# Performance work log

Hardware: AMD Instinct MI355X
Metric: run time of the kernel (lower is better)

The kernel has to match this reference:

```python
import jax, jax.numpy as jnp
import numpy as np

DIMS = (8, 8, 16, 16)   # 4D lattice, prod = 16384 sites
ND = len(DIMS)
N_IN = 4
N_OUT = 4
NC = 3
KERNEL_SIZE = 2
DILATION = 0
INIT_W = 1.0

W_IN = 2 * N_IN + 1                                  # 9
T_W = 2 * (N_IN * (KERNEL_SIZE - 1) * ND) + 1        # 33


def cconj(w):
    # swap matrix indices (axes 3,4) and negate imaginary part (last axis)
    wT = jnp.swapaxes(w, 3, 4)
    return wT * jnp.array([1.0, -1.0], dtype=w.dtype)


def complex_einsum(pattern, a, b, conj_a=1, conj_b=1):
    aR, aI = a[..., 0], conj_a * a[..., 1]
    bR, bI = b[..., 0], conj_b * b[..., 1]
    cR = jnp.einsum(pattern, aR, bR) - jnp.einsum(pattern, aI, bI)
    cI = jnp.einsum(pattern, aR, bI) + jnp.einsum(pattern, aI, bR)
    return jnp.stack((cR, cI), axis=-1)


def shift(a, axis, orientation):
    # dim 1 is flattened lattice; unflatten, roll along lattice axis, re-flatten
    o_s = a.shape
    n_s = (o_s[0],) + DIMS + o_s[2:]
    return jnp.roll(a.reshape(n_s), orientation, axis=axis + 1).reshape(o_s)


def transport(u, w, axis):
    # positive-orientation gauge transport: U w(x+mu) U^dagger
    ws = shift(w, axis, -1)
    ua = u[:, :, axis]                                 # [b, x, nc, nc, 2]
    wt = complex_einsum('bxij,bxwjk->bxwik', ua, ws)
    wt = complex_einsum('bxwij,bxkj->bxwik', wt, ua, conj_b=-1)
    return wt


def setup_inputs() -> dict:
    key = jax.random.key(0)
    k1, k2 = jax.random.split(key)
    n_sites = int(np.prod(DIMS))
    x = jax.random.normal(k1, (1, n_sites, ND + N_IN, NC, NC, 2), dtype=jnp.float32)
    std = INIT_W * np.sqrt(1.0 / (W_IN * T_W))
    weight = jax.random.normal(k2, (N_OUT, W_IN, T_W), dtype=jnp.float32) * std
    return {"x": x, "weight": weight}


def reference(x, weight):
    u, w = x[:, :, :ND], x[:, :, ND:]
    transported = []
    for axis in range(ND):
        wt = w
        for d in range(1, KERNEL_SIZE):
            for _ in range(DILATION + 1):
                wt = transport(u, wt, axis)
            transported.append(wt)
    t_w = jnp.concatenate(transported, axis=2)          # [b, x, n_in*(K-1)*ND, nc, nc, 2]

    w_full = jnp.concatenate([w, cconj(w)], axis=2)
    t_w_full = jnp.concatenate([t_w, cconj(t_w)], axis=2)

    # unit element channel
    unit = jnp.stack((jnp.eye(NC, dtype=x.dtype), jnp.zeros((NC, NC), dtype=x.dtype)), axis=-1)
    b, n_sites = x.shape[0], x.shape[1]
    unit_t = jnp.broadcast_to(unit[None, None, None], (b, n_sites, 1, NC, NC, 2))
    w_full = jnp.concatenate([w_full, unit_t], axis=2)       # [b, x, 9, nc, nc, 2]
    t_w_full = jnp.concatenate([t_w_full, unit_t], axis=2)   # [b, x, 33, nc, nc, 2]

    # bilinear gauge-covariant products, then weight contraction
    ww = complex_einsum('bxvij,bxwjk->bxvwik', w_full, t_w_full)  # [b, x, 9, 33, nc, nc, 2]
    w_out = jnp.einsum('uvw,bxvwijc->bxuijc', weight, ww)         # [b, x, n_out, nc, nc, 2]

    return jnp.concatenate([u, w_out], axis=2)
```

## Files before the change

### kernel.cpp

```cpp
#include <hip/hip_runtime.h>
#include <stdint.h>


#define SPB 16
#define TPB 256
#define NSITES 16384
#define TS2_SITE 146
#define NWGT 1188

__device__ __forceinline__ float2 pk_fma(float2 a, float2 b, float2 c){
    return make_float2(fmaf(a.x, b.x, c.x), fmaf(a.y, b.y, c.y));
}
__device__ __forceinline__ float2 spl(float s){ return make_float2(s, s); }
__device__ __forceinline__ float2 pn(float s){ return make_float2(s, -s); }
__device__ __forceinline__ float2 np(float s){ return make_float2(-s, s); }
__device__ __forceinline__ float2 swp(float2 a){ return make_float2(a.y, a.x); }

__device__ __forceinline__ int neigh(int s, int a){
    if (a == 3) return (s & ~15)        | ((s + 1)    & 15);
    if (a == 2) return (s & ~(15 << 4)) | ((s + 16)   & (15 << 4));
    if (a == 1) return (s & ~(7 << 8))  | ((s + 256)  & (7 << 8));
    return              (s & ~(7 << 11))| ((s + 2048) & (7 << 11));
}

__global__ __launch_bounds__(TPB, 2)
void gcm_fused(const float* __restrict__ xp,
               const float* __restrict__ wgt,
               float* __restrict__ outp)
{
    __shared__ float2 lt[SPB * TS2_SITE];
    __shared__ float wsm[NWGT];
    const float2* x2 = (const float2*)xp;
    float2* o2 = (float2*)outp;

    const int tid = threadIdx.x;
    const int g   = tid & 3;
    const int u   = (tid >> 2) & 3;
    const int sl  = tid >> 4;
    const int s   = blockIdx.x * SPB + sl;

    #pragma unroll 1
    for (int idx = tid; idx < NWGT; idx += TPB) wsm[idx] = wgt[idx];

    {
        const int a = u, i = g;
        float2 uc[9], wc[9];
        {
            const float2* up = x2 + (s * 8 + a) * 9;
            #pragma unroll
            for (int e = 0; e < 9; e++) uc[e] = up[e];
        }
        const int sn = neigh(s, a);
        {
            const float2* wp = x2 + (sn * 8 + 4 + i) * 9;
            #pragma unroll
            for (int e = 0; e < 9; e++) wc[e] = wp[e];
        }
        float2 t1[9];
        #pragma unroll
        for (int r = 0; r < 3; r++){
            #pragma unroll
            for (int k = 0; k < 3; k++){
                float2 acc = make_float2(0.f, 0.f);
                #pragma unroll
                for (int j = 0; j < 3; j++){
                    float2 a_ = uc[r*3+j], b_ = wc[j*3+k];
                    acc = pk_fma(spl(a_.x), b_, acc);
                    acc = pk_fma(np(a_.y), swp(b_), acc);
                }
                t1[r*3+k] = acc;
            }
        }
        float2* dst = &lt[sl * TS2_SITE + (a * 4 + i) * 9];
        #pragma unroll
        for (int r = 0; r < 3; r++){
            #pragma unroll
            for (int k = 0; k < 3; k++){
                float2 acc = make_float2(0.f, 0.f);
                #pragma unroll
                for (int j = 0; j < 3; j++){
                    float2 a_ = t1[r*3+j], b_ = uc[k*3+j];
                    acc = pk_fma(pn(a_.x), b_, acc);
                    acc = pk_fma(spl(a_.y), swp(b_), acc);
                }
                dst[r*3+k] = acc;
            }
        }
    }
    __syncthreads();

    if (g == 1){
        const float2* src = x2 + (s * 8 + u) * 9;
        float2* dst = o2 + (s * 8 + u) * 9;
        #pragma unroll
        for (int e = 0; e < 9; e++) dst[e] = src[e];
    }

    float2 M1[9], M2[9], cc[9];
    #pragma unroll
    for (int e = 0; e < 9; e++){
        M1[e] = make_float2(0.f, 0.f);
        M2[e] = make_float2(0.f, 0.f);
        cc[e] = make_float2(0.f, 0.f);
    }

    const float* wu  = wsm + u * 297;
    const float* wuA = wu + g * 33;
    const float* wuB = wu + (4 + g) * 33;
    const float* wu8 = wu + 8 * 33;

    const float2* tbase = &lt[sl * TS2_SITE];

    #pragma unroll 1
    for (int w16 = 0; w16 < 16; w16++){
        const float2* tp = tbase + w16 * 9;
        float2 tc[9];
        #pragma unroll
        for (int e = 0; e < 9; e++) tc[e] = tp[e];
        float a1 = wuA[w16], b1 = wuA[16 + w16];
        float a2 = wuB[w16], b2 = wuB[16 + w16];
        const bool mine = ((w16 >> 2) == g);
        float c8 = mine ? wu8[w16]      : 0.f;
        float d8 = mine ? wu8[16 + w16] : 0.f;
        #pragma unroll
        for (int i = 0; i < 3; i++){
            #pragma unroll
            for (int j = 0; j < 3; j++){
                const int e = i*3+j, eT = j*3+i;
                M1[e] = pk_fma(spl(a1), tc[e],  M1[e]);
                M1[e] = pk_fma(pn(b1),  tc[eT], M1[e]);
                M2[e] = pk_fma(spl(a2), tc[e],  M2[e]);
                M2[e] = pk_fma(pn(b2),  tc[eT], M2[e]);
                cc[e] = pk_fma(spl(c8), tc[e],  cc[e]);
                cc[e] = pk_fma(pn(d8),  tc[eT], cc[e]);
            }
        }
    }

    {
        float c1 = wuA[32], c2 = wuB[32];
        M1[0].x += c1; M1[4].x += c1; M1[8].x += c1;
        M2[0].x += c2; M2[4].x += c2; M2[8].x += c2;
        if (g == 0){
            float e8 = wu8[32];
            cc[0].x += e8; cc[4].x += e8; cc[8].x += e8;
        }
    }

    float2 wg[9];
    {
        const float2* wp = x2 + (s * 8 + 4 + g) * 9;
        #pragma unroll
        for (int e = 0; e < 9; e++) wg[e] = wp[e];
    }

    #pragma unroll
    for (int i = 0; i < 3; i++){
        #pragma unroll
        for (int k = 0; k < 3; k++){
            float2 acc = cc[i*3+k];
            #pragma unroll
            for (int j = 0; j < 3; j++){
                float2 a_ = wg[i*3+j];
                float2 m  = M1[j*3+k];
                acc = pk_fma(spl(a_.x), m,      acc);
                acc = pk_fma(np(a_.y),  swp(m), acc);
            }
            #pragma unroll
            for (int j = 0; j < 3; j++){
                float2 b_ = wg[j*3+i];
                float2 m  = M2[j*3+k];
                acc = pk_fma(spl(b_.x), m,      acc);
                acc = pk_fma(pn(b_.y),  swp(m), acc);
            }
            cc[i*3+k] = acc;
        }
    }

    #pragma unroll
    for (int e = 0; e < 9; e++){
        cc[e].x += __shfl_xor(cc[e].x, 1);
        cc[e].x += __shfl_xor(cc[e].x, 2);
        cc[e].y += __shfl_xor(cc[e].y, 1);
        cc[e].y += __shfl_xor(cc[e].y, 2);
    }
    if (g == 0){
        float2* dst = o2 + (s * 8 + 4 + u) * 9;
        #pragma unroll
        for (int e = 0; e < 9; e++) dst[e] = cc[e];
    }
}

extern "C" void kernel_launch(void* const* d_in, const int* in_sizes, int n_in,
                              void* d_out, int out_size, void* d_ws, size_t ws_size,
                              hipStream_t stream)
{
    const float* x = (const float*)d_in[0];
    const float* w = (const float*)d_in[1];
    float* out = (float*)d_out;
    dim3 grid(NSITES / SPB);
    dim3 block(TPB);
    hipLaunchKernelGGL(gcm_fused, grid, block, 0, stream, x, w, out);
}
```

Baseline: 76.83 us.

## Split per-output work across eight lanes per site and use native packed FMA

```diff
diff --git a/kernel.cpp b/kernel.cpp
--- a/kernel.cpp
+++ b/kernel.cpp
@@ -2,19 +2,32 @@
 #include <stdint.h>
 
 
-#define SPB 16
+typedef float v2f __attribute__((ext_vector_type(2)));
+
+#define SPB 8
 #define TPB 256
 #define NSITES 16384
 #define TS2_SITE 146
 #define NWGT 1188
 
-__device__ __forceinline__ float2 pk_fma(float2 a, float2 b, float2 c){
-    return make_float2(fmaf(a.x, b.x, c.x), fmaf(a.y, b.y, c.y));
-}
-__device__ __forceinline__ float2 spl(float s){ return make_float2(s, s); }
-__device__ __forceinline__ float2 pn(float s){ return make_float2(s, -s); }
-__device__ __forceinline__ float2 np(float s){ return make_float2(-s, s); }
-__device__ __forceinline__ float2 swp(float2 a){ return make_float2(a.y, a.x); }
+#if defined(__has_builtin)
+#if __has_builtin(__builtin_elementwise_fma)
+#define HAVE_EW_FMA 1
+#endif
+#endif
+
+__device__ __forceinline__ v2f pkfma(v2f a, v2f b, v2f c){
+#ifdef HAVE_EW_FMA
+    return __builtin_elementwise_fma(a, b, c);
+#else
+    v2f r; r.x = fmaf(a.x, b.x, c.x); r.y = fmaf(a.y, b.y, c.y); return r;
+#endif
+}
+__device__ __forceinline__ v2f spl(float s){ return (v2f){s, s}; }
+__device__ __forceinline__ v2f pn (float s){ return (v2f){s, -s}; }
+__device__ __forceinline__ v2f np (float s){ return (v2f){-s, s}; }
+__device__ __forceinline__ v2f swp(v2f a){ return __builtin_shufflevector(a, a, 1, 0); }
+__device__ __forceinline__ v2f zero2(){ return (v2f){0.f, 0.f}; }
 
 __device__ __forceinline__ int neigh(int s, int a){
     if (a == 3) return (s & ~15)        | ((s + 1)    & 15);
@@ -23,155 +36,162 @@
     return              (s & ~(7 << 11))| ((s + 2048) & (7 << 11));
 }
 
-__global__ __launch_bounds__(TPB, 2)
+__global__ __launch_bounds__(TPB, 3)
 void gcm_fused(const float* __restrict__ xp,
                const float* __restrict__ wgt,
                float* __restrict__ outp)
 {
-    __shared__ float2 lt[SPB * TS2_SITE];
+    __shared__ v2f lt[SPB * TS2_SITE];
     __shared__ float wsm[NWGT];
-    const float2* x2 = (const float2*)xp;
-    float2* o2 = (float2*)outp;
+    const v2f* x2 = (const v2f*)xp;
+    v2f* o2 = (v2f*)outp;
 
     const int tid = threadIdx.x;
-    const int g   = tid & 3;
-    const int u   = (tid >> 2) & 3;
-    const int sl  = tid >> 4;
+    const int h   = tid & 7;
+    const int u   = (tid >> 3) & 3;
+    const int sl  = tid >> 5;
     const int s   = blockIdx.x * SPB + sl;
+    const int g   = h & 3;
 
     #pragma unroll 1
     for (int idx = tid; idx < NWGT; idx += TPB) wsm[idx] = wgt[idx];
 
-    {
-        const int a = u, i = g;
-        float2 uc[9], wc[9];
+    if (h < 4){
+        v2f uc[9], wc[9];
         {
-            const float2* up = x2 + (s * 8 + a) * 9;
+            const v2f* up = x2 + (s * 8 + u) * 9;
             #pragma unroll
             for (int e = 0; e < 9; e++) uc[e] = up[e];
         }
-        const int sn = neigh(s, a);
+        const int sn = neigh(s, u);
         {
-            const float2* wp = x2 + (sn * 8 + 4 + i) * 9;
+            const v2f* wp = x2 + (sn * 8 + 4 + h) * 9;
             #pragma unroll
             for (int e = 0; e < 9; e++) wc[e] = wp[e];
         }
-        float2 t1[9];
+        v2f t1[9];
         #pragma unroll
         for (int r = 0; r < 3; r++){
             #pragma unroll
             for (int k = 0; k < 3; k++){
-                float2 acc = make_float2(0.f, 0.f);
+                v2f acc = zero2();
                 #pragma unroll
                 for (int j = 0; j < 3; j++){
-                    float2 a_ = uc[r*3+j], b_ = wc[j*3+k];
-                    acc = pk_fma(spl(a_.x), b_, acc);
-                    acc = pk_fma(np(a_.y), swp(b_), acc);
+                    v2f a_ = uc[r*3+j], b_ = wc[j*3+k];
+                    acc = pkfma(spl(a_.x), b_, acc);
+                    acc = pkfma(np(a_.y), swp(b_), acc);
                 }
                 t1[r*3+k] = acc;
             }
         }
-        float2* dst = &lt[sl * TS2_SITE + (a * 4 + i) * 9];
+        v2f* dst = &lt[sl * TS2_SITE + (u * 4 + h) * 9];
         #pragma unroll
         for (int r = 0; r < 3; r++){
             #pragma unroll
             for (int k = 0; k < 3; k++){
-                float2 acc = make_float2(0.f, 0.f);
+                v2f acc = zero2();
                 #pragma unroll
                 for (int j = 0; j < 3; j++){
-                    float2 a_ = t1[r*3+j], b_ = uc[k*3+j];
-                    acc = pk_fma(pn(a_.x), b_, acc);
-                    acc = pk_fma(spl(a_.y), swp(b_), acc);
+                    v2f a_ = t1[r*3+j], b_ = uc[k*3+j];
+                    acc = pkfma(pn(a_.x), b_, acc);
+                    acc = pkfma(spl(a_.y), swp(b_), acc);
                 }
                 dst[r*3+k] = acc;
             }
         }
+    } else if (h == 4){
+        const v2f* src = x2 + (s * 8 + u) * 9;
+        v2f* dst = o2 + (s * 8 + u) * 9;
+        #pragma unroll
+        for (int e = 0; e < 9; e++) dst[e] = src[e];
     }
     __syncthreads();
 
-    if (g == 1){
-        const float2* src = x2 + (s * 8 + u) * 9;
-        float2* dst = o2 + (s * 8 + u) * 9;
-        #pragma unroll
-        for (int e = 0; e < 9; e++) dst[e] = src[e];
-    }
-
-    float2 M1[9], M2[9], cc[9];
-    #pragma unroll
-    for (int e = 0; e < 9; e++){
-        M1[e] = make_float2(0.f, 0.f);
-        M2[e] = make_float2(0.f, 0.f);
-        cc[e] = make_float2(0.f, 0.f);
-    }
+    v2f M[9], cc[9];
+    #pragma unroll
+    for (int e = 0; e < 9; e++){ M[e] = zero2(); cc[e] = zero2(); }
 
     const float* wu  = wsm + u * 297;
-    const float* wuA = wu + g * 33;
-    const float* wuB = wu + (4 + g) * 33;
+    const float* wvh = wu + h * 33;
     const float* wu8 = wu + 8 * 33;
 
-    const float2* tbase = &lt[sl * TS2_SITE];
+    const v2f* tbase = &lt[sl * TS2_SITE];
 
     #pragma unroll 1
     for (int w16 = 0; w16 < 16; w16++){
-        const float2* tp = tbase + w16 * 9;
-        float2 tc[9];
+        const v2f* tp = tbase + w16 * 9;
+        v2f tc[9];
         #pragma unroll
         for (int e = 0; e < 9; e++) tc[e] = tp[e];
-        float a1 = wuA[w16], b1 = wuA[16 + w16];
-        float a2 = wuB[w16], b2 = wuB[16 + w16];
-        const bool mine = ((w16 >> 2) == g);
-        float c8 = mine ? wu8[w16]      : 0.f;
-        float d8 = mine ? wu8[16 + w16] : 0.f;
+        float a = wvh[w16], b = wvh[16 + w16];
         #pragma unroll
         for (int i = 0; i < 3; i++){
             #pragma unroll
             for (int j = 0; j < 3; j++){
                 const int e = i*3+j, eT = j*3+i;
-                M1[e] = pk_fma(spl(a1), tc[e],  M1[e]);
-                M1[e] = pk_fma(pn(b1),  tc[eT], M1[e]);
-                M2[e] = pk_fma(spl(a2), tc[e],  M2[e]);
-                M2[e] = pk_fma(pn(b2),  tc[eT], M2[e]);
-                cc[e] = pk_fma(spl(c8), tc[e],  cc[e]);
-                cc[e] = pk_fma(pn(d8),  tc[eT], cc[e]);
+                M[e] = pkfma(spl(a), tc[e],  M[e]);
+                M[e] = pkfma(pn(b),  tc[eT], M[e]);
+            }
+        }
+    }
+
+    #pragma unroll
+    for (int q = 0; q < 2; q++){
+        const int w16 = 2 * h + q;
+        const v2f* tp = tbase + w16 * 9;
+        v2f tc[9];
+        #pragma unroll
+        for (int e = 0; e < 9; e++) tc[e] = tp[e];
+        float c8 = wu8[w16], d8 = wu8[16 + w16];
+        #pragma unroll
+        for (int i = 0; i < 3; i++){
+            #pragma unroll
+            for (int j = 0; j < 3; j++){
+                const int e = i*3+j, eT = j*3+i;
+                cc[e] = pkfma(spl(c8), tc[e],  cc[e]);
+                cc[e] = pkfma(pn(d8),  tc[eT], cc[e]);
             }
         }
     }
 
     {
-        float c1 = wuA[32], c2 = wuB[32];
-        M1[0].x += c1; M1[4].x += c1; M1[8].x += c1;
-        M2[0].x += c2; M2[4].x += c2; M2[8].x += c2;
-        if (g == 0){
+        float ch = wvh[32];
+        M[0].x += ch; M[4].x += ch; M[8].x += ch;
+        if (h == 0){
             float e8 = wu8[32];
             cc[0].x += e8; cc[4].x += e8; cc[8].x += e8;
         }
     }
 
-    float2 wg[9];
+    v2f A[9];
     {
-        const float2* wp = x2 + (s * 8 + 4 + g) * 9;
-        #pragma unroll
-        for (int e = 0; e < 9; e++) wg[e] = wp[e];
+        const v2f* wp = x2 + (s * 8 + 4 + g) * 9;
+        v2f wgr[9];
+        #pragma unroll
+        for (int e = 0; e < 9; e++) wgr[e] = wp[e];
+        const bool dag = (h >= 4);
+        #pragma unroll
+        for (int i = 0; i < 3; i++){
+            #pragma unroll
+            for (int j = 0; j < 3; j++){
+                v2f p = wgr[i*3+j];
+                v2f q = wgr[j*3+i]; q.y = -q.y;
+                A[i*3+j] = dag ? q : p;
+            }
+        }
     }
 
     #pragma unroll
     for (int i = 0; i < 3; i++){
         #pragma unroll
         for (int k = 0; k < 3; k++){
-            float2 acc = cc[i*3+k];
-            #pragma unroll
-            for (int j = 0; j < 3; j++){
-                float2 a_ = wg[i*3+j];
-                float2 m  = M1[j*3+k];
-                acc = pk_fma(spl(a_.x), m,      acc);
-                acc = pk_fma(np(a_.y),  swp(m), acc);
-            }
-            #pragma unroll
-            for (int j = 0; j < 3; j++){
-                float2 b_ = wg[j*3+i];
-                float2 m  = M2[j*3+k];
-                acc = pk_fma(spl(b_.x), m,      acc);
-                acc = pk_fma(pn(b_.y),  swp(m), acc);
+            v2f acc = cc[i*3+k];
+            #pragma unroll
+            for (int j = 0; j < 3; j++){
+                v2f a_ = A[i*3+j];
+                v2f m  = M[j*3+k];
+                acc = pkfma(spl(a_.x), m,      acc);
+                acc = pkfma(np(a_.y),  swp(m), acc);
             }
             cc[i*3+k] = acc;
         }
@@ -179,13 +199,14 @@
 
     #pragma unroll
     for (int e = 0; e < 9; e++){
-        cc[e].x += __shfl_xor(cc[e].x, 1);
-        cc[e].x += __shfl_xor(cc[e].x, 2);
-        cc[e].y += __shfl_xor(cc[e].y, 1);
-        cc[e].y += __shfl_xor(cc[e].y, 2);
-    }
-    if (g == 0){
-        float2* dst = o2 + (s * 8 + 4 + u) * 9;
+        #pragma unroll
+        for (int d = 1; d <= 4; d <<= 1){
+            cc[e].x += __shfl_xor(cc[e].x, d);
+            cc[e].y += __shfl_xor(cc[e].y, d);
+        }
+    }
+    if (h == 0){
+        v2f* dst = o2 + (s * 8 + 4 + u) * 9;
         #pragma unroll
         for (int e = 0; e < 9; e++) dst[e] = cc[e];
     }
```

Result: slower. 83.54 us (+8.7%).
